# Optimization experiments

Measured on AMD Instinct MI355X. Metric: run time of the kernel, lower is better.

The kernel has to match this reference:

```python
import jax, jax.numpy as jnp
import numpy as np

SCORE_THRESH = 0.25
NMS_THRESH = 0.45
DET_PER_IMG = 300
PRE_NMS_TOPK = 2048  # fixed-size candidate set replacing dynamic torch.where


def setup_inputs() -> dict:
    key = jax.random.key(0)
    k1, k2, k3, k4 = jax.random.split(key, 4)
    B, N, C5 = 16, 25200, 85  # YOLOv5 @640: 3*(80^2+40^2+20^2)=25200 anchors, 80 classes + 5
    head_outputs = jax.random.normal(k1, (B, N, C5), jnp.float32)
    grid = jax.random.uniform(k2, (N, 2), jnp.float32) * 80.0          # cell coords
    anchor_grid = jax.random.uniform(k3, (N, 2), jnp.float32) * 60.0 + 4.0  # anchor w/h in px
    stride = 8.0 * (1.0 + jax.random.uniform(k4, (N, 1), jnp.float32))      # per-anchor stride
    return {"head_outputs": head_outputs, "grid": grid,
            "anchor_grid": anchor_grid, "stride": stride}


def _pairwise_iou(b):
    # b: [K,4] xyxy -> [K,K] IoU
    area = (b[:, 2] - b[:, 0]) * (b[:, 3] - b[:, 1])
    lt = jnp.maximum(b[:, None, :2], b[None, :, :2])
    rb = jnp.minimum(b[:, None, 2:], b[None, :, 2:])
    wh = jnp.clip(rb - lt, 0.0)
    inter = wh[..., 0] * wh[..., 1]
    return inter / (area[:, None] + area[None, :] - inter + 1e-7)


def _nms_keep(boxes, valid, thr):
    # boxes sorted by descending score; greedy suppression via scan
    K = boxes.shape[0]
    iou = _pairwise_iou(boxes)
    def body(keep, i):
        row = jnp.where(keep[i], iou[i] <= thr, True)  # i suppresses overlapping j only if kept
        row = row.at[i].set(keep[i])                   # never self-suppress
        return keep & row, None
    keep, _ = jax.lax.scan(body, valid, jnp.arange(K))
    return keep


def _postprocess_single(head, grid, anchor_grid, stride):
    p = jax.nn.sigmoid(head)                     # [N, 85]
    scores = p[:, 5:] * p[:, 4:5]                # [N, C] class * objectness
    N, C = scores.shape
    # BoxCoder.decode_single (cxcywh -> xyxy)
    xy = (p[:, :2] * 2.0 - 0.5 + grid) * stride  # [N,2]
    wh = (p[:, 2:4] * 2.0) ** 2 * anchor_grid    # [N,2]
    boxes = jnp.concatenate([xy - wh * 0.5, xy + wh * 0.5], axis=1)  # [N,4]

    # torch.where(scores > thresh) -> fixed-size top-k over flattened (anchor, class)
    flat = jnp.where(scores > SCORE_THRESH, scores, -1.0).reshape(-1)
    top_s, top_i = jax.lax.top_k(flat, PRE_NMS_TOPK)
    a_idx = top_i // C
    labels = (top_i % C).astype(jnp.int32)
    cand = boxes[a_idx]                          # [K,4]
    valid = top_s > 0.0

    # batched_nms: per-class coordinate offset so classes never overlap
    offset = (jnp.max(cand) + 1.0) * labels.astype(cand.dtype)[:, None]
    keep = _nms_keep(cand + offset, valid, NMS_THRESH)

    kept_s = jnp.where(keep, top_s, -1.0)
    fs, fi = jax.lax.top_k(kept_s, DET_PER_IMG)  # keep[:detections_per_img]
    ok = fs > 0.0
    fb = jnp.where(ok[:, None], cand[fi], 0.0)
    fl = jnp.where(ok, labels[fi], -1)
    return fb, fs, fl


def reference(head_outputs, grid, anchor_grid, stride):
    boxes, scores, labels = jax.vmap(
        lambda h: _postprocess_single(h, grid, anchor_grid, stride))(head_outputs)
    # padded analogue of List[Dict]: boxes [B,300,4], scores [B,300], labels [B,300]
    return boxes, scores, labels
```

## Files before the change

### kernel.cpp

```cpp
#include <hip/hip_runtime.h>
#include <hip/hip_bf16.h>

#define B    16
#define NA   25200
#define NCH  85
#define NCLS 80
#define K    2048
#define CAP  4096
#define ACAP 4096
#define DET  300
#define TILE 64
#define NTILES 394
#define PBLK 64
#define LBUF 2304
#define SBASE  0x3FD0000000000000ULL
#define SSHIFT 42

typedef unsigned long long u64;
typedef unsigned int u32;
typedef unsigned short u16;
typedef unsigned char u8;

__device__ __forceinline__ double dsig(float x) { return 1.0 / (1.0 + exp(-(double)x)); }
__device__ __forceinline__ float  fsig(float x) { return 1.0f / (1.0f + __expf(-x)); }

__global__ void __launch_bounds__(256) k_hist(const float* __restrict__ head,
                                              u32* __restrict__ phist, u16* __restrict__ smax16) {
    __shared__ float rows[TILE * NCH];
    __shared__ int h[2048];
    __shared__ float smaxT[TILE][4];
    int tid = threadIdx.x;
    int hblk = gridDim.x;
    for (int i = tid; i < 2048; i += 256) h[i] = 0;
    int img = blockIdx.y;
    const float* ibase = head + (size_t)img * NA * NCH;

    float4 pf[6];
    int tile = blockIdx.x;
    {
        int a0 = tile * TILE;
        int na = NA - a0; if (na > TILE) na = TILE;
        int nf4 = (na * NCH) >> 2;
        const float4* src = (const float4*)(ibase + (size_t)a0 * NCH);
        #pragma unroll
        for (int u = 0; u < 6; ++u) { int i = tid + u * 256; pf[u] = (i < nf4) ? src[i] : make_float4(0.f,0.f,0.f,0.f); }
    }
    for (; tile < NTILES; tile += hblk) {
        int a0 = tile * TILE;
        int na = NA - a0; if (na > TILE) na = TILE;
        int nf4 = (na * NCH) >> 2;
        __syncthreads();
        #pragma unroll
        for (int u = 0; u < 6; ++u) { int i = tid + u * 256; if (i < nf4) ((float4*)rows)[i] = pf[u]; }
        __syncthreads();
        int nt = tile + hblk;
        if (nt < NTILES) {
            int a0n = nt * TILE;
            int nan_ = NA - a0n; if (nan_ > TILE) nan_ = TILE;
            int nf4n = (nan_ * NCH) >> 2;
            const float4* srcn = (const float4*)(ibase + (size_t)a0n * NCH);
            #pragma unroll
            for (int u = 0; u < 6; ++u) { int i = tid + u * 256; pf[u] = (i < nf4n) ? srcn[i] : make_float4(0.f,0.f,0.f,0.f); }
        }
        for (int t = tid; t < 4 * na; t += 256) {
            int a = t >> 2, q = t & 3;
            float fo = fsig(rows[a * NCH + 4]);
            float lm = 0.0f;
            if (fo > 0.25f) {
                float qq = 0.24975f / fo;
                float cth = __logf(qq) - __logf(1.0f - qq);
                int c0 = q * 20;
                for (int c = c0; c < c0 + 20; ++c) {
                    float cl = rows[a * NCH + 5 + c];
                    if (cl > cth) {
                        float sc = fo * fsig(cl);
                        lm = fmaxf(lm, sc);
                        if (sc > 0.25f) {
                            u64 bits = (u64)__double_as_longlong((double)sc);
                            int bb = (int)((bits - SBASE) >> SSHIFT);
                            if (bb > 2047) bb = 2047;
                            atomicAdd(&h[bb], 1);
                        }
                    }
                }
            }
            smaxT[a][q] = lm;
        }
        __syncthreads();
        for (int t = tid; t < na; t += 256) {
            float m = fmaxf(fmaxf(smaxT[t][0], smaxT[t][1]), fmaxf(smaxT[t][2], smaxT[t][3]));
            u32 mb = __float_as_uint(m);
            smax16[(size_t)img * NA + a0 + t] = (u16)((mb + 0xFFFFu) >> 16);
        }
    }
    __syncthreads();
    u32* dst = phist + ((size_t)img * hblk + blockIdx.x) * 2048;
    for (int i = tid; i < 2048; i += 256) dst[i] = (u32)h[i];
}

__global__ void __launch_bounds__(256) k_redsum(const u32* __restrict__ phist,
                                                int* __restrict__ hist, int hblk,
                                                u32* __restrict__ cnt, u32* __restrict__ cntA) {
    int img = blockIdx.x;
    int bin = blockIdx.y * 256 + threadIdx.x;
    if (blockIdx.y == 0 && threadIdx.x == 0) cnt[img] = 0;
    if (blockIdx.y == 0 && threadIdx.x == 1) cntA[img] = 0;
    const u32* base = phist + (size_t)img * hblk * 2048 + bin;
    u32 s = 0;
    int p = 0;
    for (; p + 4 <= hblk; p += 4) {
        u32 a0 = base[(size_t)(p + 0) * 2048];
        u32 a1 = base[(size_t)(p + 1) * 2048];
        u32 a2 = base[(size_t)(p + 2) * 2048];
        u32 a3 = base[(size_t)(p + 3) * 2048];
        s += a0 + a1 + a2 + a3;
    }
    for (; p < hblk; ++p) s += base[(size_t)p * 2048];
    hist[img * 2048 + bin] = (int)s;
}

__global__ void __launch_bounds__(1024) k_cut(const int* __restrict__ hist, u64* __restrict__ cut) {
    int lane = threadIdx.x & 63;
    int img  = threadIdx.x >> 6;
    const int* h = hist + img * 2048;
    int v[32];
    #pragma unroll
    for (int ch = 0; ch < 32; ++ch) v[ch] = h[2047 - ch * 64 - lane];
    int cum = 0; u64 cb = 0;
    #pragma unroll
    for (int ch = 0; ch < 32; ++ch) {
        int pfx = v[ch];
        for (int d = 1; d < 64; d <<= 1) { int o = __shfl_up(pfx, d, 64); if (lane >= d) pfx += o; }
        u64 ball = __ballot(cum + pfx >= K);
        if (ball) {
            int fl = __ffsll((long long)ball) - 1;
            int bin = 2047 - ch * 64 - fl;
            cb = (bin >= 1) ? (SBASE + ((u64)(bin - 1) << SSHIFT)) : 0ULL;
            break;
        }
        cum += __shfl(pfx, 63, 64);
    }
    if (lane == 0) cut[img] = cb;
}

__global__ void __launch_bounds__(256) k_screen(const u16* __restrict__ smax16, const u64* __restrict__ cut,
                                                u32* __restrict__ cntA, int* __restrict__ alist) {
    __shared__ int lcnt, lbase, buf[256];
    int img = blockIdx.y;
    int a = blockIdx.x * 256 + threadIdx.x;
    if (threadIdx.x == 0) lcnt = 0;
    __syncthreads();
    u64 cutb = cut[img];
    float cutf = cutb ? (float)__longlong_as_double((long long)cutb) : 0.25f;
    float pre = fmaxf(0.2489f, cutf * 0.999f);
    if (a < NA) {
        float fup = __uint_as_float(((u32)smax16[(size_t)img * NA + a]) << 16);
        if (fup >= pre) buf[atomicAdd(&lcnt, 1)] = a;
    }
    __syncthreads();
    if (threadIdx.x == 0 && lcnt) lbase = atomicAdd(&cntA[img], (u32)lcnt);
    __syncthreads();
    for (int i = threadIdx.x; i < lcnt; i += 256) {
        int pos = lbase + i;
        if (pos < ACAP) alist[img * ACAP + pos] = buf[i];
    }
}

__global__ void __launch_bounds__(256) k_pairs(const float* __restrict__ head, const u64* __restrict__ cut,
                                               const float* __restrict__ grid, const float* __restrict__ ag,
                                               const float* __restrict__ stv,
                                               const u32* __restrict__ cntA, const int* __restrict__ alist,
                                               u32* __restrict__ cnt, u64* __restrict__ sb, u32* __restrict__ si,
                                               double* __restrict__ boxg) {
    __shared__ u64 lsb[LBUF];
    __shared__ u32 lsi[LBUF];
    __shared__ u32 lcnt, lbase;
    int img = blockIdx.y;
    int tid = threadIdx.x;
    u64 cutb = cut[img];
    float cutf = cutb ? (float)__longlong_as_double((long long)cutb) : 0.25f;
    float pre = fmaxf(0.2489f, cutf * 0.999f);
    int nsur = (int)cntA[img]; if (nsur > ACAP) nsur = ACAP;
    int npairs = nsur * NCLS;
    u64* sbi = sb + (size_t)img * CAP;
    u32* sii = si + (size_t)img * CAP;
    const float* ibase = head + (size_t)img * NA * NCH;
    if (tid == 0) lcnt = 0;
    __syncthreads();

    int base = blockIdx.x * 256;
    int ntrip = (npairs > base) ? (npairs - base + PBLK * 256 - 1) / (PBLK * 256) : 0;
    for (int t = 0; t <= ntrip; ++t) {
        if (t < ntrip) {
            int p = base + tid + t * PBLK * 256;
            if (p < npairs) {
                int ai = (int)((u32)p / NCLS);
                int c  = p - ai * NCLS;
                int a  = alist[img * ACAP + ai];
                const float* row = ibase + (size_t)a * NCH;
                float o = row[4], cl = row[5 + c];
                float s32 = fsig(o) * fsig(cl);
                if (s32 >= pre) {
                    double sc = dsig(o) * dsig(cl);
                    if (sc > 0.25) {
                        u64 bits = (u64)__double_as_longlong(sc);
                        if (bits >= cutb) {
                            u32 pos = atomicAdd(&lcnt, 1u);
                            if (pos < LBUF) { lsb[pos] = bits; lsi[pos] = (u32)(a * NCLS + c); }
                        }
                    }
                }
            }
        }
        __syncthreads();
        bool last = (t == ntrip);
        if ((!last && lcnt >= 2048) || (last && lcnt > 0)) {
            u32 n = lcnt; if (n > LBUF) n = LBUF;
            if (tid == 0) lbase = atomicAdd(&cnt[img], n);
            __syncthreads();
            for (u32 i = tid; i < n; i += 256) {
                u32 pos = lbase + i;
                if (pos < CAP) {
                    u32 idx = lsi[i];
                    sbi[pos] = lsb[i]; sii[pos] = idx;
                    int a = (int)(idx / NCLS);
                    const float* row = ibase + (size_t)a * NCH;
                    double p0 = dsig(row[0]), p1 = dsig(row[1]), p2 = dsig(row[2]), p3 = dsig(row[3]);
                    double st = (double)stv[a];
                    double xc = (p0 * 2.0 - 0.5 + (double)grid[a * 2 + 0]) * st;
                    double yc = (p1 * 2.0 - 0.5 + (double)grid[a * 2 + 1]) * st;
                    double w = p2 * 2.0; w = (w * w) * (double)ag[a * 2 + 0];
                    double h = p3 * 2.0; h = (h * h) * (double)ag[a * 2 + 1];
                    double* bg = boxg + ((size_t)img * CAP + pos) * 4;
                    bg[0] = xc - w * 0.5; bg[1] = yc - h * 0.5;
                    bg[2] = xc + w * 0.5; bg[3] = yc + h * 0.5;
                }
            }
            __syncthreads();
            if (tid == 0) lcnt = 0;
            __syncthreads();
        }
    }
}

__global__ void __launch_bounds__(1024) k_sortp(const u32* __restrict__ cntArr,
                                                u64* __restrict__ sb, u32* __restrict__ si,
                                                u16* __restrict__ permg, u8* __restrict__ keptg,
                                                int* __restrict__ violg) {
    __shared__ u64 TA[4096];
    __shared__ u32 TI[4096];
    __shared__ u16 TP[4096];
    __shared__ u32 h2[2048];
    __shared__ u32 cntb[2048];
    __shared__ u32 segtot[32];
    int img = blockIdx.x;
    int tid = threadIdx.x;
    int lane = tid & 63, wv = tid >> 6;
    u32* tmp = TI;

    u64* A = sb + (size_t)img * CAP;
    u32* I = si + (size_t)img * CAP;
    int cnt = (int)cntArr[img]; if (cnt > CAP) cnt = CAP;

    keptg[(size_t)img * 2048 + tid] = 1;
    keptg[(size_t)img * 2048 + 1024 + tid] = 1;
    if (tid == 0) violg[img] = 0;

    for (int b = tid; b < 2048; b += 1024) h2[b] = 0;
    __syncthreads();
    for (int e = tid; e < cnt; e += 1024) {
        u64 bits = A[e];
        int b = (int)((bits - SBASE) >> SSHIFT);
        b = b < 0 ? 0 : (b > 2047 ? 2047 : b);
        atomicAdd(&h2[b], 1u);
    }
    __syncthreads();
    for (int s = wv; s < 32; s += 16) {
        int r = s * 64 + lane;
        u32 v = h2[2047 - r];
        cntb[2047 - r] = v;
        u32 p = v;
        for (int d = 1; d < 64; d <<= 1) { u32 o = __shfl_up(p, d, 64); if (lane >= d) p += o; }
        if (lane == 63) segtot[s] = p;
        tmp[r] = p - v;
    }
    __syncthreads();
    if (tid < 32) {
        u32 v = segtot[tid], p = v;
        for (int d = 1; d < 32; d <<= 1) { u32 o = __shfl_up(p, d, 64); if (lane >= d) p += o; }
        segtot[tid] = p - v;
    }
    __syncthreads();
    for (int s = wv; s < 32; s += 16) {
        int r = s * 64 + lane;
        h2[2047 - r] = tmp[r] + segtot[s];
    }
    __syncthreads();
    for (int e = tid; e < 4096; e += 1024) if (e >= cnt) { TA[e] = 0ULL; TI[e] = 0xFFFFFFFFu; TP[e] = 0; }
    __syncthreads();
    for (int e = tid; e < cnt; e += 1024) {
        u64 bits = A[e]; u32 idx = I[e];
        int b = (int)((bits - SBASE) >> SSHIFT);
        b = b < 0 ? 0 : (b > 2047 ? 2047 : b);
        u32 slot = atomicAdd(&h2[b], 1u);
        if (slot < 4096u) { TA[slot] = bits; TI[slot] = idx; TP[slot] = (u16)e; }
    }
    __syncthreads();
    u64 rb[4]; u32 ri[4]; int rp[4]; u16 rq[4];
    #pragma unroll
    for (int s4 = 0; s4 < 4; ++s4) {
        int p = tid + s4 * 1024;
        rp[s4] = -1;
        if (p < cnt) {
            u64 kb = TA[p]; u32 ki = TI[p]; u16 kq = TP[p];
            int b = (int)((kb - SBASE) >> SSHIFT);
            b = b < 0 ? 0 : (b > 2047 ? 2047 : b);
            int en = (int)h2[b];
            int st = en - (int)cntb[b];
            int r = st;
            for (int j = st; j < en; ++j) {
                u64 b2 = TA[j]; u32 i2 = TI[j];
                if (b2 > kb || (b2 == kb && i2 < ki)) ++r;
            }
            rb[s4] = kb; ri[s4] = ki; rq[s4] = kq; rp[s4] = r;
        }
    }
    __syncthreads();
    #pragma unroll
    for (int s4 = 0; s4 < 4; ++s4)
        if (rp[s4] >= 0 && rp[s4] < 4096) { TA[rp[s4]] = rb[s4]; TI[rp[s4]] = ri[s4]; TP[rp[s4]] = rq[s4]; }
    __syncthreads();
    A[tid] = TA[tid];               I[tid] = TI[tid];
    A[1024 + tid] = TA[1024 + tid]; I[1024 + tid] = TI[1024 + tid];
    permg[(size_t)img * 2048 + tid]        = TP[tid];
    permg[(size_t)img * 2048 + 1024 + tid] = TP[1024 + tid];
}

#define NMS_FRONT_HALF                                                          \
    u64 sv[2]; u32 fidx[2];                                                     \
    sv[0] = A[tid];        fidx[0] = I[tid];                                    \
    sv[1] = A[1024 + tid]; fidx[1] = I[1024 + tid];                             \
    if (tid < NCLS) clscnt[tid] = 0;                                            \
    for (int i = tid; i < 32 * NCLS; i += 1024) ((u32*)chunkcnt)[i] = 0;        \
    double bx[2][4];                                                            \
    int lab[2];                                                                 \
    bool val[2];                                                                \
    double lmax = -1e300, lmin = 1e300;                                         \
    __syncthreads();                                                            \
    _Pragma("unroll")                                                           \
    for (int q = 0; q < 2; ++q) {                                               \
        int slot = q * 1024 + tid;                                              \
        val[q] = (sv[q] != 0ULL);                                               \
        bx[q][0] = bx[q][1] = bx[q][2] = bx[q][3] = 0.0;                        \
        lab[q] = 0;                                                             \
        if (val[q]) {                                                           \
            lab[q] = (int)(fidx[q] % NCLS);                                     \
            int p = (int)permg[(size_t)img * 2048 + slot];                      \
            const double* bg = boxg + ((size_t)img * CAP + p) * 4;              \
            bx[q][0] = bg[0]; bx[q][1] = bg[1];                                 \
            bx[q][2] = bg[2]; bx[q][3] = bg[3];                                 \
            lmax = fmax(lmax, fmax(fmax(bx[q][0], bx[q][1]), fmax(bx[q][2], bx[q][3]))); \
            lmin = fmin(lmin, fmin(fmin(bx[q][0], bx[q][1]), fmin(bx[q][2], bx[q][3]))); \
            atomicAdd(&clscnt[lab[q]], 1);                                      \
            atomicAdd(&chunkcnt[slot >> 6][lab[q]], 1u);                        \
        }                                                                       \
        labs[slot] = val[q] ? (u16)lab[q] : (u16)0xFFFF;                        \
    }                                                                           \
    for (int d = 1; d < 64; d <<= 1) {                                          \
        lmax = fmax(lmax, __shfl_xor(lmax, d, 64));                             \
        lmin = fmin(lmin, __shfl_xor(lmin, d, 64));                             \
    }                                                                           \
    if (lane == 0) { red[wv] = lmax; red2[wv] = lmin; }                         \
    __syncthreads();                                                            \
    if (tid == 0) {                                                             \
        double m = red[0], mn = red2[0];                                        \
        for (int w2 = 1; w2 < 16; ++w2) { m = fmax(m, red[w2]); mn = fmin(mn, red2[w2]); } \
        s_offb = m + 1.0;                                                       \
        s_viol2 = (m + 2.0 + mn < 0.0) ? 1 : 0;                                 \
    }                                                                           \
    __syncthreads();                                                            \
    double offb = s_offb;                                                       \
    double oB[2][4], aR[2];                                                     \
    _Pragma("unroll")                                                           \
    for (int q = 0; q < 2; ++q) {                                               \
        double off = offb * (double)lab[q];                                     \
        oB[q][0] = bx[q][0] + off; oB[q][1] = bx[q][1] + off;                   \
        oB[q][2] = bx[q][2] + off; oB[q][3] = bx[q][3] + off;                   \
        aR[q] = (oB[q][2] - oB[q][0]) * (oB[q][3] - oB[q][1]);                  \
        int slot = q * 1024 + tid;                                              \
        obm[0][slot] = oB[q][0]; obm[1][slot] = oB[q][1];                       \
        obm[2][slot] = oB[q][2]; obm[3][slot] = oB[q][3];                       \
    }                                                                           \
    __syncthreads();                                                            \
    if (tid < 64) {                                                             \
        int c0 = clscnt[lane];                                                  \
        int c1 = (lane < NCLS - 64) ? clscnt[64 + lane] : 0;                    \
        int p0 = c0;                                                            \
        for (int d = 1; d < 64; d <<= 1) { int o = __shfl_up(p0, d, 64); if (lane >= d) p0 += o; } \
        int tot0 = __shfl(p0, 63, 64);                                          \
        int p1 = c1;                                                            \
        for (int d = 1; d < 64; d <<= 1) { int o = __shfl_up(p1, d, 64); if (lane >= d) p1 += o; } \
        clsbase[lane] = p0 - c0;                                                \
        if (lane < NCLS - 64) clsbase[64 + lane] = tot0 + p1 - c1;              \
        if (lane == 63) clsbase[NCLS] = tot0 + __shfl(p1, NCLS - 64 - 1, 64);   \
    }                                                                           \
    __syncthreads();                                                            \
    if (tid < NCLS) {                                                           \
        int running = clsbase[tid];                                             \
        for (int ch = 0; ch < 32; ++ch) {                                       \
            u32 t = chunkcnt[ch][tid];                                          \
            chunkcnt[ch][tid] = (u32)running;                                   \
            running += (int)t;                                                  \
        }                                                                       \
    }                                                                           \
    __syncthreads();                                                            \
    _Pragma("unroll")                                                           \
    for (int q = 0; q < 2; ++q) {                                               \
        int cl = val[q] ? lab[q] : -1;                                          \
        int rank = 0;                                                           \
        for (int d = 1; d < 64; ++d) {                                          \
            int oc = __shfl_up(cl, d, 64);                                      \
            if (lane >= d && oc == cl) ++rank;                                  \
        }                                                                       \
        if (val[q]) {                                                           \
            int slot = q * 1024 + tid;                                          \
            seg[chunkcnt[slot >> 6][cl] + rank] = (u16)slot;                    \
        }                                                                       \
    }                                                                           \
    __syncthreads();

__global__ void __launch_bounds__(1024) k_greedy(const u64* __restrict__ sb, const u32* __restrict__ si,
        const u16* __restrict__ permg, const double* __restrict__ boxg,
        u8* __restrict__ keptg, int* __restrict__ violg) {
    __shared__ double obm[4][K];
    __shared__ u16 labs[K];
    __shared__ u16 seg[K];
    __shared__ u32 chunkcnt[32][NCLS];
    __shared__ int clsbase[NCLS + 1];
    __shared__ int clscnt[NCLS];
    __shared__ double red[16], red2[16];
    __shared__ double s_offb;
    __shared__ int s_viol2;
    __shared__ u64 amw[16][32];

    int img = blockIdx.x;
    int tid = threadIdx.x;
    int lane = tid & 63, wv = tid >> 6;
    const u64* A = sb + (size_t)img * CAP;
    const u32* I = si + (size_t)img * CAP;

    NMS_FRONT_HALF

    if (tid == 0 && s_viol2) atomicOr(&violg[img], 1);

    int c = blockIdx.y * 16 + wv;
    int cbase = clsbase[c];
    int m = clsbase[c + 1] - cbase;
    u8* kp = keptg + (size_t)img * 2048;
    if (m > 1) {
        if (m <= 64) {
            int s_l = (lane < m) ? (int)seg[cbase + lane] : -1;
            double e0 = 0, e1 = 0, e2 = 0, e3 = 0, ea = 0;
            if (s_l >= 0) {
                e0 = obm[0][s_l]; e1 = obm[1][s_l];
                e2 = obm[2][s_l]; e3 = obm[3][s_l];
                ea = (e2 - e0) * (e3 - e1);
            }
            u64 ovl = 0ULL;
            for (int k = 0; k < m; ++k) {
                double k0 = __shfl(e0, k, 64), k1 = __shfl(e1, k, 64);
                double k2 = __shfl(e2, k, 64), k3 = __shfl(e3, k, 64);
                double ka = __shfl(ea, k, 64);
                double ww = fmax(fmin(k2, e2) - fmax(k0, e0), 0.0);
                double hh = fmax(fmin(k3, e3) - fmax(k1, e1), 0.0);
                double inter = ww * hh;
                bool o = (lane > k) && (lane < m) &&
                         (inter > 0.45 * (ka + ea - inter + 1e-7));
                ovl |= o ? (1ULL << k) : 0ULL;
            }
            u64 live = (m >= 64) ? ~0ULL : ((1ULL << m) - 1ULL);
            for (int k = 0; k < m; ++k) {
                u64 kill = __ballot((ovl >> k) & 1ULL);
                if ((live >> k) & 1ULL) live &= ~kill;
            }
            if (s_l >= 0 && !((live >> lane) & 1ULL)) kp[s_l] = 0;
        } else {
            u64* AM = amw[wv];
            if (lane < 32) {
                int lo = lane * 64;
                AM[lane] = (m >= lo + 64) ? ~0ULL : (m > lo ? ((1ULL << (m - lo)) - 1ULL) : 0ULL);
            }
            for (int k = 0; k < m; ++k) {
                if (!((AM[k >> 6] >> (k & 63)) & 1ULL)) continue;
                int sk = (int)seg[cbase + k];
                double k0 = obm[0][sk], k1 = obm[1][sk];
                double k2 = obm[2][sk], k3 = obm[3][sk];
                double ka = (k2 - k0) * (k3 - k1);
                for (int j = k + 1 + lane; j < m; j += 64) {
                    if (!((AM[j >> 6] >> (j & 63)) & 1ULL)) continue;
                    int t = (int)seg[cbase + j];
                    double b0 = obm[0][t], b1 = obm[1][t];
                    double b2 = obm[2][t], b3 = obm[3][t];
                    double ww = fmax(fmin(k2, b2) - fmax(k0, b0), 0.0);
                    double hh = fmax(fmin(k3, b3) - fmax(k1, b1), 0.0);
                    double inter = ww * hh;
                    double aj = (b2 - b0) * (b3 - b1);
                    if (inter > 0.45 * (ka + aj - inter + 1e-7))
                        atomicAnd(&AM[j >> 6], ~(1ULL << (j & 63)));
                }
            }
            for (int j = lane; j < m; j += 64)
                if (!((AM[j >> 6] >> (j & 63)) & 1ULL)) kp[(int)seg[cbase + j]] = 0;
        }
    }

    {
        int cend = cbase + m;
        bool bad = false;
        for (int ii = cbase + lane; ii < cend; ii += 64) {
            int s = (int)seg[ii];
            float c0 = (float)obm[0][s], c1 = (float)obm[1][s];
            float c2v = (float)obm[2][s], c3 = (float)obm[3][s];
            float ca = (c2v - c0) * (c3 - c1);
            #pragma unroll
            for (int dd = 0; dd < 2; ++dd) {
                int cc = c + (dd ? 1 : -1);
                if (cc < 0 || cc >= NCLS) continue;
                int je = clsbase[cc + 1];
                for (int j = clsbase[cc]; j < je; ++j) {
                    int t = (int)seg[j];
                    if (t > s) {
                        float b0 = (float)obm[0][t], b1 = (float)obm[1][t];
                        float b2 = (float)obm[2][t], b3 = (float)obm[3][t];
                        float ww = fmaxf(fminf(c2v, b2) - fmaxf(c0, b0), 0.f);
                        float hh = fmaxf(fminf(c3, b3) - fmaxf(c1, b1), 0.f);
                        float inter = ww * hh;
                        float aj = (b2 - b0) * (b3 - b1);
                        if (inter > 0.4485f * (ca + aj - inter + 1e-7f)) bad = true;
                    }
                }
            }
        }
        if (__ballot(bad)) { if (lane == 0) atomicOr(&violg[img], 1); }
    }
}

__global__ void __launch_bounds__(1024) k_fin(const u64* __restrict__ sb, const u32* __restrict__ si,
        const u16* __restrict__ permg, const double* __restrict__ boxg,
        const u8* __restrict__ keptg, const int* __restrict__ violg, float* __restrict__ out) {
    __shared__ double obm[4][K];
    __shared__ u16 labs[K];
    __shared__ u16 seg[K];
    __shared__ u32 chunkcnt[32][NCLS];
    __shared__ int clsbase[NCLS + 1];
    __shared__ int clscnt[NCLS];
    __shared__ double red[16], red2[16];
    __shared__ double s_offb;
    __shared__ int s_viol2;
    __shared__ u64 mask[32];
    __shared__ int wpfx[33];

    int img = blockIdx.x;
    int tid = threadIdx.x;
    int lane = tid & 63, wv = tid >> 6;
    const u64* A = sb + (size_t)img * CAP;
    const u32* I = si + (size_t)img * CAP;

    float* bo  = out + (size_t)img * DET * 4;
    float* so_ = out + (size_t)B * DET * 4 + (size_t)img * DET;
    float* lo  = out + (size_t)B * DET * 5 + (size_t)img * DET;

    if (violg[img] == 0) {
        u64 s0 = A[tid], s1 = A[1024 + tid];
        u32 f0 = I[tid], f1 = I[1024 + tid];
        const u8* kp = keptg + (size_t)img * 2048;
        bool k0 = (s0 != 0ULL) && (kp[tid] != 0);
        bool k1 = (s1 != 0ULL) && (kp[1024 + tid] != 0);
        u64 m0 = __ballot(k0), m1 = __ballot(k1);
        if (lane == 0) { mask[wv] = m0; mask[16 + wv] = m1; }
        __syncthreads();
        if (tid == 0) {
            int s = 0;
            for (int w2 = 0; w2 < 32; ++w2) { wpfx[w2] = s; s += __popcll(mask[w2]); }
            wpfx[32] = s;
        }
        __syncthreads();
        int total = wpfx[32]; if (total > DET) total = DET;
        #pragma unroll
        for (int q = 0; q < 2; ++q) {
            int slot = q * 1024 + tid;
            int w = slot >> 6, bpos = slot & 63;
            if ((mask[w] >> bpos) & 1ULL) {
                int r = wpfx[w] + __popcll(mask[w] & ((1ULL << bpos) - 1ULL));
                if (r < DET) {
                    int p = (int)permg[(size_t)img * 2048 + slot];
                    const double* bg = boxg + ((size_t)img * CAP + p) * 4;
                    bo[r * 4 + 0] = (float)bg[0]; bo[r * 4 + 1] = (float)bg[1];
                    bo[r * 4 + 2] = (float)bg[2]; bo[r * 4 + 3] = (float)bg[3];
                    u64 sv_ = q ? s1 : s0;
                    u32 fi_ = q ? f1 : f0;
                    so_[r] = (float)__longlong_as_double((long long)sv_);
                    lo[r] = (float)(fi_ % NCLS);
                }
            }
        }
        if (tid >= total && tid < DET) {
            bo[tid * 4 + 0] = 0.f; bo[tid * 4 + 1] = 0.f;
            bo[tid * 4 + 2] = 0.f; bo[tid * 4 + 3] = 0.f;
            so_[tid] = -1.0f; lo[tid] = -1.0f;
        }
        return;
    }

    NMS_FRONT_HALF

    {
        u64 v0 = __ballot(val[0]), v1 = __ballot(val[1]);
        if (lane == 0) { mask[wv] = v0; mask[16 + wv] = v1; }
    }
    bool alive[2]; alive[0] = val[0]; alive[1] = val[1];
    __syncthreads();
    int i = -1, kc = 0;
    while (true) {
        int start = i + 1;
        if (start >= K) break;
        int w = start >> 6;
        u64 m = mask[w] & (~0ULL << (start & 63));
        while (m == 0ULL) { if (++w >= 32) break; m = mask[w]; }
        if (w >= 32) break;
        i = (w << 6) + __ffsll((long long)m) - 1;
        ++kc;
        if (kc >= DET) break;
        double bi0 = obm[0][i], bi1 = obm[1][i];
        double bi2 = obm[2][i], bi3 = obm[3][i];
        double ai = (bi2 - bi0) * (bi3 - bi1);
        #pragma unroll
        for (int q = 0; q < 2; ++q) {
            int slot = q * 1024 + tid;
            double w_ = fmax(fmin(bi2, oB[q][2]) - fmax(bi0, oB[q][0]), 0.0);
            double h_ = fmax(fmin(bi3, oB[q][3]) - fmax(bi1, oB[q][1]), 0.0);
            double inter = w_ * h_;
            bool sup = inter > 0.45 * (ai + aR[q] - inter + 1e-7);
            if (alive[q] && slot > i && sup) {
                alive[q] = false;
                atomicAnd(&mask[slot >> 6], ~(1ULL << (slot & 63)));
            }
        }
        __syncthreads();
    }
    __syncthreads();

    if (tid == 0) {
        int s = 0;
        for (int w2 = 0; w2 < 32; ++w2) { wpfx[w2] = s; s += __popcll(mask[w2]); }
        wpfx[32] = s;
    }
    __syncthreads();
    int total = wpfx[32]; if (total > DET) total = DET;

    #pragma unroll
    for (int q = 0; q < 2; ++q) {
        int slot = q * 1024 + tid;
        int w = slot >> 6, bpos = slot & 63;
        if ((mask[w] >> bpos) & 1ULL) {
            int r = wpfx[w] + __popcll(mask[w] & ((1ULL << bpos) - 1ULL));
            if (r < DET) {
                bo[r * 4 + 0] = (float)bx[q][0]; bo[r * 4 + 1] = (float)bx[q][1];
                bo[r * 4 + 2] = (float)bx[q][2]; bo[r * 4 + 3] = (float)bx[q][3];
                so_[r] = (float)__longlong_as_double((long long)sv[q]);
                lo[r] = (float)lab[q];
            }
        }
    }
    if (tid >= total && tid < DET) {
        bo[tid * 4 + 0] = 0.f; bo[tid * 4 + 1] = 0.f;
        bo[tid * 4 + 2] = 0.f; bo[tid * 4 + 3] = 0.f;
        so_[tid] = -1.0f; lo[tid] = -1.0f;
    }
}

extern "C" void kernel_launch(void* const* d_in, const int* in_sizes, int n_in,
                              void* d_out, int out_size, void* d_ws, size_t ws_size,
                              hipStream_t stream) {
    const float* head = (const float*)d_in[0];
    const float* grid = (const float*)d_in[1];
    const float* ag   = (const float*)d_in[2];
    const float* stv  = (const float*)d_in[3];
    float* out = (float*)d_out;
    char* ws = (char*)d_ws;

    u64* sb     = (u64*)(ws + 0);
    u32* si     = (u32*)(ws + 524288);
    int* alist  = (int*)(ws + 786432);
    u16* permg  = (u16*)(ws + 786432);
    u8*  keptg  = (u8*)(ws + 851968);
    int* violg  = (int*)(ws + 884736);
    u32* cnt    = (u32*)(ws + 1048576);
    u32* cntA   = (u32*)(ws + 1048640);
    u64* cut    = (u64*)(ws + 1048704);
    u16* smax16 = (u16*)(ws + 1048832);
    int* hist   = (int*)(ws + 1855232);
    u32* phist  = (u32*)(ws + 1986304);
    double* boxg = (double*)(ws + 1986304);

    int hblk = 16;
    if (ws_size >= (size_t)1986304 + (size_t)B * 128 * 2048 * 4) hblk = 128;
    else if (ws_size >= (size_t)1986304 + (size_t)B * 64 * 2048 * 4) hblk = 64;

    k_hist   <<<dim3(hblk, B), 256, 0, stream>>>(head, phist, smax16);
    k_redsum <<<dim3(B, 8), 256, 0, stream>>>(phist, hist, hblk, cnt, cntA);
    k_cut    <<<1, 1024, 0, stream>>>(hist, cut);
    k_screen <<<dim3((NA + 255) / 256, B), 256, 0, stream>>>(smax16, cut, cntA, alist);
    k_pairs  <<<dim3(PBLK, B), 256, 0, stream>>>(head, cut, grid, ag, stv, cntA, alist, cnt, sb, si, boxg);
    k_sortp  <<<B, 1024, 0, stream>>>(cnt, sb, si, permg, keptg, violg);
    k_greedy <<<dim3(B, 5), 1024, 0, stream>>>(sb, si, permg, boxg, keptg, violg);
    k_fin    <<<B, 1024, 0, stream>>>(sb, si, permg, boxg, keptg, violg, out);
}
```

Measured before the change: 154.9 us.

## Move class segmentation into sort kernel and drop redundant front half from greedy

The per-class bucketing (class counts, prefix bases, segment order), the max-coordinate offset and the offset-validity check now run once per image at the end of the sort kernel and are written to workspace. The greedy NMS kernel no longer redoes that shared-memory setup in each of its 5 blocks per image. It reads boxes directly from global memory through the permutation and adds the class offset on the fly. This removes duplicated setup work and large shared allocations in the greedy kernel, at the cost of extra work in the single-block-per-image sort kernel and uncached global reads in the inner loops.

```diff
diff --git a/kernel.cpp b/kernel.cpp
--- a/kernel.cpp
+++ b/kernel.cpp
@@ -246,13 +246,20 @@
 __global__ void __launch_bounds__(1024) k_sortp(const u32* __restrict__ cntArr,
                                                 u64* __restrict__ sb, u32* __restrict__ si,
                                                 u16* __restrict__ permg, u8* __restrict__ keptg,
-                                                int* __restrict__ violg) {
+                                                int* __restrict__ violg,
+                                                const double* __restrict__ boxg,
+                                                u16* __restrict__ segg, int* __restrict__ clsbg,
+                                                double* __restrict__ offbg) {
     __shared__ u64 TA[4096];
     __shared__ u32 TI[4096];
     __shared__ u16 TP[4096];
     __shared__ u32 h2[2048];
     __shared__ u32 cntb[2048];
     __shared__ u32 segtot[32];
+    __shared__ u32 chunkcnt[32][NCLS];
+    __shared__ int clsbase[NCLS + 1];
+    __shared__ int clscnt[NCLS];
+    __shared__ double redA[16], redB[16];
     int img = blockIdx.x;
     int tid = threadIdx.x;
     int lane = tid & 63, wv = tid >> 6;
@@ -334,6 +341,76 @@
     A[1024 + tid] = TA[1024 + tid]; I[1024 + tid] = TI[1024 + tid];
     permg[(size_t)img * 2048 + tid]        = TP[tid];
     permg[(size_t)img * 2048 + 1024 + tid] = TP[1024 + tid];
+
+    if (tid < NCLS) clscnt[tid] = 0;
+    for (int i = tid; i < 32 * NCLS; i += 1024) ((u32*)chunkcnt)[i] = 0;
+    __syncthreads();
+    int lab_[2]; bool val_[2];
+    double lmax = -1e300, lmin = 1e300;
+    #pragma unroll
+    for (int q = 0; q < 2; ++q) {
+        int slot = q * 1024 + tid;
+        val_[q] = (TA[slot] != 0ULL);
+        lab_[q] = 0;
+        if (val_[q]) {
+            lab_[q] = (int)(TI[slot] % NCLS);
+            const double* bg = boxg + ((size_t)img * CAP + TP[slot]) * 4;
+            double b0 = bg[0], b1 = bg[1], b2 = bg[2], b3 = bg[3];
+            lmax = fmax(lmax, fmax(fmax(b0, b1), fmax(b2, b3)));
+            lmin = fmin(lmin, fmin(fmin(b0, b1), fmin(b2, b3)));
+            atomicAdd(&clscnt[lab_[q]], 1);
+            atomicAdd(&chunkcnt[slot >> 6][lab_[q]], 1u);
+        }
+    }
+    for (int d = 1; d < 64; d <<= 1) {
+        lmax = fmax(lmax, __shfl_xor(lmax, d, 64));
+        lmin = fmin(lmin, __shfl_xor(lmin, d, 64));
+    }
+    if (lane == 0) { redA[wv] = lmax; redB[wv] = lmin; }
+    __syncthreads();
+    if (tid == 0) {
+        double m_ = redA[0], mn = redB[0];
+        for (int w2 = 1; w2 < 16; ++w2) { m_ = fmax(m_, redA[w2]); mn = fmin(mn, redB[w2]); }
+        offbg[img] = m_ + 1.0;
+        if (m_ + 2.0 + mn < 0.0) atomicOr(&violg[img], 1);
+    }
+    __syncthreads();
+    if (tid < 64) {
+        int c0 = clscnt[lane];
+        int c1 = (lane < NCLS - 64) ? clscnt[64 + lane] : 0;
+        int p0 = c0;
+        for (int d = 1; d < 64; d <<= 1) { int o = __shfl_up(p0, d, 64); if (lane >= d) p0 += o; }
+        int tot0 = __shfl(p0, 63, 64);
+        int p1 = c1;
+        for (int d = 1; d < 64; d <<= 1) { int o = __shfl_up(p1, d, 64); if (lane >= d) p1 += o; }
+        clsbase[lane] = p0 - c0;
+        if (lane < NCLS - 64) clsbase[64 + lane] = tot0 + p1 - c1;
+        if (lane == 63) clsbase[NCLS] = tot0 + __shfl(p1, NCLS - 64 - 1, 64);
+    }
+    __syncthreads();
+    if (tid < NCLS) {
+        int running = clsbase[tid];
+        for (int ch = 0; ch < 32; ++ch) {
+            u32 t = chunkcnt[ch][tid];
+            chunkcnt[ch][tid] = (u32)running;
+            running += (int)t;
+        }
+    }
+    for (int i = tid; i <= NCLS; i += 1024) clsbg[img * 81 + i] = clsbase[i];
+    __syncthreads();
+    #pragma unroll
+    for (int q = 0; q < 2; ++q) {
+        int cl = val_[q] ? lab_[q] : -1;
+        int rank = 0;
+        for (int d = 1; d < 64; ++d) {
+            int oc = __shfl_up(cl, d, 64);
+            if (lane >= d && oc == cl) ++rank;
+        }
+        if (val_[q]) {
+            int slot = q * 1024 + tid;
+            segg[(size_t)img * 2048 + chunkcnt[slot >> 6][cl] + rank] = (u16)slot;
+        }
+    }
 }
 
 #define NMS_FRONT_HALF                                                          \
@@ -429,43 +506,35 @@
     }                                                                           \
     __syncthreads();
 
-__global__ void __launch_bounds__(1024) k_greedy(const u64* __restrict__ sb, const u32* __restrict__ si,
+__global__ void __launch_bounds__(1024) k_greedy(const u16* __restrict__ segg,
+        const int* __restrict__ clsbg, const double* __restrict__ offbg,
         const u16* __restrict__ permg, const double* __restrict__ boxg,
         u8* __restrict__ keptg, int* __restrict__ violg) {
-    __shared__ double obm[4][K];
-    __shared__ u16 labs[K];
-    __shared__ u16 seg[K];
-    __shared__ u32 chunkcnt[32][NCLS];
-    __shared__ int clsbase[NCLS + 1];
-    __shared__ int clscnt[NCLS];
-    __shared__ double red[16], red2[16];
-    __shared__ double s_offb;
-    __shared__ int s_viol2;
     __shared__ u64 amw[16][32];
-
     int img = blockIdx.x;
-    int tid = threadIdx.x;
-    int lane = tid & 63, wv = tid >> 6;
-    const u64* A = sb + (size_t)img * CAP;
-    const u32* I = si + (size_t)img * CAP;
-
-    NMS_FRONT_HALF
-
-    if (tid == 0 && s_viol2) atomicOr(&violg[img], 1);
-
+    int lane = threadIdx.x & 63, wv = threadIdx.x >> 6;
     int c = blockIdx.y * 16 + wv;
-    int cbase = clsbase[c];
-    int m = clsbase[c + 1] - cbase;
+    const int* cb_ = clsbg + img * 81;
+    int cbase = cb_[c];
+    int m = cb_[c + 1] - cbase;
+    if (m <= 0) return;
+    double offb = offbg[img];
+    double off = offb * (double)c;
+    const u16* sg = segg + (size_t)img * 2048;
+    const u16* pg = permg + (size_t)img * 2048;
+    const double* BG = boxg + (size_t)img * CAP * 4;
     u8* kp = keptg + (size_t)img * 2048;
-    if (m > 1) {
-        if (m <= 64) {
-            int s_l = (lane < m) ? (int)seg[cbase + lane] : -1;
-            double e0 = 0, e1 = 0, e2 = 0, e3 = 0, ea = 0;
-            if (s_l >= 0) {
-                e0 = obm[0][s_l]; e1 = obm[1][s_l];
-                e2 = obm[2][s_l]; e3 = obm[3][s_l];
-                ea = (e2 - e0) * (e3 - e1);
-            }
+
+    if (m <= 64) {
+        int s_l = (lane < m) ? (int)sg[cbase + lane] : -1;
+        double e0 = 0, e1 = 0, e2 = 0, e3 = 0, ea = 0;
+        if (s_l >= 0) {
+            const double* bg = BG + (size_t)pg[s_l] * 4;
+            e0 = bg[0] + off; e1 = bg[1] + off;
+            e2 = bg[2] + off; e3 = bg[3] + off;
+            ea = (e2 - e0) * (e3 - e1);
+        }
+        if (m > 1) {
             u64 ovl = 0ULL;
             for (int k = 0; k < m; ++k) {
                 double k0 = __shfl(e0, k, 64), k1 = __shfl(e1, k, 64);
@@ -484,54 +553,81 @@
                 if ((live >> k) & 1ULL) live &= ~kill;
             }
             if (s_l >= 0 && !((live >> lane) & 1ULL)) kp[s_l] = 0;
-        } else {
-            u64* AM = amw[wv];
-            if (lane < 32) {
-                int lo = lane * 64;
-                AM[lane] = (m >= lo + 64) ? ~0ULL : (m > lo ? ((1ULL << (m - lo)) - 1ULL) : 0ULL);
-            }
-            for (int k = 0; k < m; ++k) {
-                if (!((AM[k >> 6] >> (k & 63)) & 1ULL)) continue;
-                int sk = (int)seg[cbase + k];
-                double k0 = obm[0][sk], k1 = obm[1][sk];
-                double k2 = obm[2][sk], k3 = obm[3][sk];
-                double ka = (k2 - k0) * (k3 - k1);
-                for (int j = k + 1 + lane; j < m; j += 64) {
-                    if (!((AM[j >> 6] >> (j & 63)) & 1ULL)) continue;
-                    int t = (int)seg[cbase + j];
-                    double b0 = obm[0][t], b1 = obm[1][t];
-                    double b2 = obm[2][t], b3 = obm[3][t];
-                    double ww = fmax(fmin(k2, b2) - fmax(k0, b0), 0.0);
-                    double hh = fmax(fmin(k3, b3) - fmax(k1, b1), 0.0);
-                    double inter = ww * hh;
-                    double aj = (b2 - b0) * (b3 - b1);
-                    if (inter > 0.45 * (ka + aj - inter + 1e-7))
-                        atomicAnd(&AM[j >> 6], ~(1ULL << (j & 63)));
-                }
-            }
-            for (int j = lane; j < m; j += 64)
-                if (!((AM[j >> 6] >> (j & 63)) & 1ULL)) kp[(int)seg[cbase + j]] = 0;
-        }
-    }
-
-    {
-        int cend = cbase + m;
+        }
         bool bad = false;
-        for (int ii = cbase + lane; ii < cend; ii += 64) {
-            int s = (int)seg[ii];
-            float c0 = (float)obm[0][s], c1 = (float)obm[1][s];
-            float c2v = (float)obm[2][s], c3 = (float)obm[3][s];
+        if (s_l >= 0) {
+            float c0 = (float)e0, c1 = (float)e1, c2v = (float)e2, c3 = (float)e3;
             float ca = (c2v - c0) * (c3 - c1);
             #pragma unroll
             for (int dd = 0; dd < 2; ++dd) {
                 int cc = c + (dd ? 1 : -1);
                 if (cc < 0 || cc >= NCLS) continue;
-                int je = clsbase[cc + 1];
-                for (int j = clsbase[cc]; j < je; ++j) {
-                    int t = (int)seg[j];
+                double offc = offb * (double)cc;
+                int je = cb_[cc + 1];
+                for (int j = cb_[cc]; j < je; ++j) {
+                    int t = (int)sg[j];
+                    if (t > s_l) {
+                        const double* bgt = BG + (size_t)pg[t] * 4;
+                        float b0 = (float)(bgt[0] + offc), b1 = (float)(bgt[1] + offc);
+                        float b2 = (float)(bgt[2] + offc), b3 = (float)(bgt[3] + offc);
+                        float ww = fmaxf(fminf(c2v, b2) - fmaxf(c0, b0), 0.f);
+                        float hh = fmaxf(fminf(c3, b3) - fmaxf(c1, b1), 0.f);
+                        float inter = ww * hh;
+                        float aj = (b2 - b0) * (b3 - b1);
+                        if (inter > 0.4485f * (ca + aj - inter + 1e-7f)) bad = true;
+                    }
+                }
+            }
+        }
+        if (__ballot(bad)) { if (lane == 0) atomicOr(&violg[img], 1); }
+    } else {
+        u64* AM = amw[wv];
+        if (lane < 32) {
+            int lo = lane * 64;
+            AM[lane] = (m >= lo + 64) ? ~0ULL : (m > lo ? ((1ULL << (m - lo)) - 1ULL) : 0ULL);
+        }
+        for (int k = 0; k < m; ++k) {
+            if (!((AM[k >> 6] >> (k & 63)) & 1ULL)) continue;
+            int sk = (int)sg[cbase + k];
+            const double* bgk = BG + (size_t)pg[sk] * 4;
+            double k0 = bgk[0] + off, k1 = bgk[1] + off;
+            double k2 = bgk[2] + off, k3 = bgk[3] + off;
+            double ka = (k2 - k0) * (k3 - k1);
+            for (int j = k + 1 + lane; j < m; j += 64) {
+                if (!((AM[j >> 6] >> (j & 63)) & 1ULL)) continue;
+                int t = (int)sg[cbase + j];
+                const double* bgt = BG + (size_t)pg[t] * 4;
+                double b0 = bgt[0] + off, b1 = bgt[1] + off;
+                double b2 = bgt[2] + off, b3 = bgt[3] + off;
+                double ww = fmax(fmin(k2, b2) - fmax(k0, b0), 0.0);
+                double hh = fmax(fmin(k3, b3) - fmax(k1, b1), 0.0);
+                double inter = ww * hh;
+                double aj = (b2 - b0) * (b3 - b1);
+                if (inter > 0.45 * (ka + aj - inter + 1e-7))
+                    atomicAnd(&AM[j >> 6], ~(1ULL << (j & 63)));
+            }
+        }
+        for (int j = lane; j < m; j += 64)
+            if (!((AM[j >> 6] >> (j & 63)) & 1ULL)) kp[(int)sg[cbase + j]] = 0;
+        bool bad = false;
+        for (int ii = cbase + lane; ii < cbase + m; ii += 64) {
+            int s = (int)sg[ii];
+            const double* bgs = BG + (size_t)pg[s] * 4;
+            float c0 = (float)(bgs[0] + off), c1 = (float)(bgs[1] + off);
+            float c2v = (float)(bgs[2] + off), c3 = (float)(bgs[3] + off);
+            float ca = (c2v - c0) * (c3 - c1);
+            #pragma unroll
+            for (int dd = 0; dd < 2; ++dd) {
+                int cc = c + (dd ? 1 : -1);
+                if (cc < 0 || cc >= NCLS) continue;
+                double offc = offb * (double)cc;
+                int je = cb_[cc + 1];
+                for (int j = cb_[cc]; j < je; ++j) {
+                    int t = (int)sg[j];
                     if (t > s) {
-                        float b0 = (float)obm[0][t], b1 = (float)obm[1][t];
-                        float b2 = (float)obm[2][t], b3 = (float)obm[3][t];
+                        const double* bgt = BG + (size_t)pg[t] * 4;
+                        float b0 = (float)(bgt[0] + offc), b1 = (float)(bgt[1] + offc);
+                        float b2 = (float)(bgt[2] + offc), b3 = (float)(bgt[3] + offc);
                         float ww = fmaxf(fminf(c2v, b2) - fmaxf(c0, b0), 0.f);
                         float hh = fmaxf(fminf(c3, b3) - fmaxf(c1, b1), 0.f);
                         float inter = ww * hh;
@@ -695,6 +791,9 @@
     u16* permg  = (u16*)(ws + 786432);
     u8*  keptg  = (u8*)(ws + 851968);
     int* violg  = (int*)(ws + 884736);
+    u16* segg   = (u16*)(ws + 917504);
+    int* clsbg  = (int*)(ws + 983040);
+    double* offbg = (double*)(ws + 988288);
     u32* cnt    = (u32*)(ws + 1048576);
     u32* cntA   = (u32*)(ws + 1048640);
     u64* cut    = (u64*)(ws + 1048704);
@@ -712,7 +811,7 @@
     k_cut    <<<1, 1024, 0, stream>>>(hist, cut);
     k_screen <<<dim3((NA + 255) / 256, B), 256, 0, stream>>>(smax16, cut, cntA, alist);
     k_pairs  <<<dim3(PBLK, B), 256, 0, stream>>>(head, cut, grid, ag, stv, cntA, alist, cnt, sb, si, boxg);
-    k_sortp  <<<B, 1024, 0, stream>>>(cnt, sb, si, permg, keptg, violg);
-    k_greedy <<<dim3(B, 5), 1024, 0, stream>>>(sb, si, permg, boxg, keptg, violg);
+    k_sortp  <<<B, 1024, 0, stream>>>(cnt, sb, si, permg, keptg, violg, boxg, segg, clsbg, offbg);
+    k_greedy <<<dim3(B, 5), 1024, 0, stream>>>(segg, clsbg, offbg, permg, boxg, keptg, violg);
     k_fin    <<<B, 1024, 0, stream>>>(sb, si, permg, boxg, keptg, violg, out);
 }
```

Measured after the change: 167.4 us. +8.1%, slower.
